# Kernel optimization log

Hardware: AMD Instinct MI355X
Metric: run time of the kernel (lower is better)

The kernel has to match this reference:

```python
import jax, jax.numpy as jnp
import numpy as np

D_MODEL = 512
NUM_HEADS = 8


def setup_inputs() -> dict:
    key = jax.random.key(0)
    ks = jax.random.split(key, 6)
    B, S, D = 4, 2048, D_MODEL
    Q = jax.random.normal(ks[0], (B, S, D), dtype=jnp.float32)
    K = jax.random.normal(ks[1], (B, S, D), dtype=jnp.float32)
    V = jax.random.normal(ks[2], (B, S, D), dtype=jnp.float32)
    # boolean mask, True = masked out; random so no row is fully masked
    mask = jax.random.randint(ks[3], (B, S, S), 0, 2).astype(jnp.bool_)
    scale = 1.0 / np.sqrt(D)
    Wq = jax.random.normal(ks[4], (D, D), dtype=jnp.float32) * scale
    Wo = jax.random.normal(ks[5], (D, D), dtype=jnp.float32) * scale
    return {"Q": Q, "K": K, "V": V, "mask": mask, "Wq": Wq, "Wo": Wo}


def reference(Q, K, V, mask, Wq, Wo):
    B, S, D = Q.shape
    H = NUM_HEADS
    dk = D // H
    # Faithful to the source: Q_Linear's weight (Wq) is applied to Q, K AND V
    # (K_Linear / V_Linear are dead parameters in the original module).
    q = (Q @ Wq.T).reshape(B, S, H, dk)
    k = (K @ Wq.T).reshape(B, S, H, dk)
    v = (V @ Wq.T).reshape(B, S, H, dk)
    # scores: [B, H, Sq, Sk]
    scores = jnp.einsum("bqhd,bkhd->bhqk", q, k)
    scores = jnp.where(mask[:, None, :, :], -jnp.inf, scores)
    w = jax.nn.softmax(scores / jnp.sqrt(jnp.asarray(dk, scores.dtype)), axis=-1)
    c = jnp.einsum("bhqk,bkhd->bqhd", w, v).reshape(B, S, D)
    return c @ Wo.T
```

## Files before the change

kernel.cpp:

```cpp
#include <hip/hip_runtime.h>
#include <math.h>

#define B_ 4
#define S_ 2048
#define D_ 512
#define H_ 8
#define DK_ 64
#define MROWS (B_ * S_)

typedef short bf16x8 __attribute__((ext_vector_type(8)));
typedef float f32x4 __attribute__((ext_vector_type(4)));
typedef float f32x16 __attribute__((ext_vector_type(16)));

static __device__ __forceinline__ unsigned short f2bf(float x) {
    unsigned int u = __float_as_uint(x);
    return (unsigned short)((u + 0x7FFFu + ((u >> 16) & 1u)) >> 16);
}
static __device__ __forceinline__ unsigned int cvt_pk_bf16(float a, float b) {
    unsigned int r;
    asm("v_cvt_pk_bf16_f32 %0, %1, %2" : "=v"(r) : "v"(a), "v"(b));
    return r;
}
static __device__ __forceinline__ float exp2_fast(float x) {
    float r;
    asm("v_exp_f32 %0, %1" : "=v"(r) : "v"(x));
    return r;
}
static __device__ __forceinline__ void gld_lds16(const unsigned short* g, unsigned short* l) {
    __builtin_amdgcn_global_load_lds(
        (const __attribute__((address_space(1))) unsigned int*)g,
        (__attribute__((address_space(3))) unsigned int*)l, 16, 0, 0);
}
static __device__ __forceinline__ void plswap(unsigned int& a, unsigned int& b) {
    asm volatile("v_permlane32_swap_b32 %0, %1" : "+v"(a), "+v"(b));
}

#define NXE (MROWS * D_)
#define NWE (D_ * D_)
#define CAST_BLOCKS ((3 * NXE + 2 * NWE) / 8 / 256)
#define MASKE (B_ * S_ * S_)
#define MASK_BLOCKS (MASKE / 256 / 4)
#define MASKB_BYTE (MASKE / 256 / 16)

__global__ __launch_bounds__(256) void prep(const float* __restrict__ Q,
                                            const float* __restrict__ K,
                                            const float* __restrict__ V,
                                            const float* __restrict__ Wq,
                                            const float* __restrict__ Wo,
                                            const void* __restrict__ mask,
                                            unsigned short* __restrict__ Qb,
                                            unsigned short* __restrict__ Kb,
                                            unsigned short* __restrict__ Vb,
                                            unsigned short* __restrict__ Wqb,
                                            unsigned short* __restrict__ Wob,
                                            unsigned long long* __restrict__ mb) {
    if (blockIdx.x < CAST_BLOCKS) {
        const int NA = NXE / 8;
        const int NWn = NWE / 8;
        int id = blockIdx.x * 256 + threadIdx.x;
        const float* src;
        unsigned short* dst;
        if (id < 3 * NA) {
            int a = id / NA, r = id - a * NA;
            src = (a == 0 ? Q : a == 1 ? K : V) + (size_t)r * 8;
            dst = (a == 0 ? Qb : a == 1 ? Kb : Vb) + (size_t)r * 8;
        } else {
            int r = id - 3 * NA;
            int a = r / NWn; r -= a * NWn;
            src = (a == 0 ? Wq : Wo) + (size_t)r * 8;
            dst = (a == 0 ? Wqb : Wob) + (size_t)r * 8;
        }
        float4 x = *(const float4*)src;
        float4 y = *(const float4*)(src + 4);
        unsigned short u[8] = {f2bf(x.x), f2bf(x.y), f2bf(x.z), f2bf(x.w),
                               f2bf(y.x), f2bf(y.y), f2bf(y.z), f2bf(y.w)};
        *(uint4*)dst = *(const uint4*)u;
    } else {
        const int mblk = blockIdx.x - CAST_BLOCKS;
        unsigned int accw = 0;
        if ((threadIdx.x & 63) == 0) {
            const unsigned int* mw0 = (const unsigned int*)mask;
            #pragma unroll
            for (int i = 0; i < 16; ++i) accw |= mw0[i];
        }
        accw = __shfl(accw, 0);
        const bool bytemode = (accw & 0xFFFFFF00u) != 0u;
        if (bytemode) {
            if (mblk >= MASKB_BYTE) return;
            const int gid = mblk * 256 + threadIdx.x;
            uint4 x = ((const uint4*)mask)[gid];
            unsigned int n[4];
            const unsigned int xs[4] = {x.x, x.y, x.z, x.w};
            #pragma unroll
            for (int i = 0; i < 4; ++i) {
                unsigned int y = xs[i];
                y |= y >> 4; y |= y >> 2; y |= y >> 1;
                y &= 0x01010101u;
                n[i] = (y * 0x01020408u) >> 24;
            }
            const unsigned short piece =
                (unsigned short)(n[0] | (n[1] << 4) | (n[2] << 8) | (n[3] << 12));
            ((unsigned short*)mb)[gid] = piece;
        } else {
            const int wid = (mblk * 256 + threadIdx.x) >> 6;
            const int lane = threadIdx.x & 63;
            const unsigned int* mi = (const unsigned int*)mask;
            const size_t base = (size_t)wid * 256;
            unsigned long long b0 = __ballot(mi[base + lane] != 0);
            unsigned long long b1 = __ballot(mi[base + 64 + lane] != 0);
            unsigned long long b2 = __ballot(mi[base + 128 + lane] != 0);
            unsigned long long b3 = __ballot(mi[base + 192 + lane] != 0);
            if (lane == 0) {
                const size_t wix = base >> 6;
                mb[wix] = b0; mb[wix + 1] = b1; mb[wix + 2] = b2; mb[wix + 3] = b3;
            }
        }
    }
}

__global__ __launch_bounds__(256) void proj3(const unsigned short* __restrict__ Qb,
                                             const unsigned short* __restrict__ Kb,
                                             const unsigned short* __restrict__ Vb,
                                             const unsigned short* __restrict__ Wqb,
                                             unsigned short* __restrict__ qs,
                                             unsigned short* __restrict__ kbo,
                                             unsigned short* __restrict__ vt) {
    __shared__ unsigned short smx[16384];
    const int t = threadIdx.x;
    const int w = t >> 6, lane = t & 63, col = lane & 15, quad = lane >> 4;
    const int bm = blockIdx.x * 128, bn = blockIdx.y * 128;
    const int z = blockIdx.z;
    const unsigned short* X = (z == 0) ? Qb : (z == 1) ? Kb : Vb;
    const int wm = (w >> 1) * 64, wn = (w & 1) * 64;

    const int sr = w * 32 + (lane >> 2);
    const int ssw = (((lane & 3) ^ ((lane >> 3) & 3)) * 8);
    const unsigned short* ags = X + (size_t)(bm + sr) * D_ + ssw;
    const unsigned short* bgs = Wqb + (size_t)(bn + sr) * D_ + ssw;
    const int pseg = ((quad ^ ((col >> 1) & 3)) * 8);

    f32x4 acc[4][4];
    #pragma unroll
    for (int i = 0; i < 4; ++i)
        #pragma unroll
        for (int j = 0; j < 4; ++j) acc[i][j] = (f32x4){0.f, 0.f, 0.f, 0.f};

    gld_lds16(ags, &smx[w * 1024]);
    gld_lds16(ags + 16 * D_, &smx[w * 1024 + 512]);
    gld_lds16(bgs, &smx[4096 + w * 1024]);
    gld_lds16(bgs + 16 * D_, &smx[4096 + w * 1024 + 512]);
    __asm__ __volatile__("s_waitcnt vmcnt(0)" ::: "memory");
    __builtin_amdgcn_s_barrier();

    int cur = 0;
    #pragma unroll 1
    for (int k0 = 0; k0 < D_; k0 += 32) {
        if (k0 + 32 < D_) {
            const int nb = (cur ^ 1) * 8192;
            gld_lds16(ags + k0 + 32, &smx[nb + w * 1024]);
            gld_lds16(ags + 16 * D_ + k0 + 32, &smx[nb + w * 1024 + 512]);
            gld_lds16(bgs + k0 + 32, &smx[nb + 4096 + w * 1024]);
            gld_lds16(bgs + 16 * D_ + k0 + 32, &smx[nb + 4096 + w * 1024 + 512]);
        }
        __builtin_amdgcn_sched_barrier(0);

        const int cb = cur * 8192;
        bf16x8 af[4], bg[4];
        #pragma unroll
        for (int i = 0; i < 4; ++i)
            af[i] = *(const bf16x8*)&smx[cb + (wm + i * 16 + col) * 32 + pseg];
        #pragma unroll
        for (int j = 0; j < 4; ++j)
            bg[j] = *(const bf16x8*)&smx[cb + 4096 + (wn + j * 16 + col) * 32 + pseg];
        #pragma unroll
        for (int i = 0; i < 4; ++i)
            #pragma unroll
            for (int j = 0; j < 4; ++j)
                acc[i][j] = __builtin_amdgcn_mfma_f32_16x16x32_bf16(
                    af[i], bg[j], acc[i][j], 0, 0, 0);

        __asm__ __volatile__("s_waitcnt vmcnt(0)" ::: "memory");
        __builtin_amdgcn_s_barrier();
        cur ^= 1;
    }

    if (z == 2) {
        #pragma unroll
        for (int i = 0; i < 4; ++i) {
            const int R = bm + wm + i * 16 + quad * 4;
            const int bb = R >> 11, s0 = R & (S_ - 1);
            #pragma unroll
            for (int j = 0; j < 4; ++j) {
                const int C = bn + wn + j * 16 + col;
                const int hh = C >> 6, dd = C & (DK_ - 1);
                ushort4 u = make_ushort4(f2bf(acc[i][j][0]), f2bf(acc[i][j][1]),
                                         f2bf(acc[i][j][2]), f2bf(acc[i][j][3]));
                *(ushort4*)&vt[(((size_t)bb * H_ + hh) * DK_ + dd) * S_ + s0] = u;
            }
        }
    } else {
        unsigned short* O = (z == 0) ? qs : kbo;
        const float scl = (z == 0) ? 0.18033688f : 1.0f;
        #pragma unroll
        for (int i = 0; i < 4; ++i)
            #pragma unroll
            for (int j = 0; j < 4; ++j) {
                const int R = bm + wm + i * 16 + quad * 4;
                const int C = bn + wn + j * 16 + col;
                #pragma unroll
                for (int r = 0; r < 4; ++r)
                    O[(size_t)(R + r) * D_ + C] = f2bf(acc[i][j][r] * scl);
            }
    }
}

__global__ __launch_bounds__(256) void gemm_out(const unsigned short* __restrict__ Xb,
                                                const unsigned short* __restrict__ Wob,
                                                float* __restrict__ Out) {
    __shared__ unsigned short smx[16384];
    const int t = threadIdx.x;
    const int w = t >> 6, lane = t & 63, col = lane & 15, quad = lane >> 4;
    const int bm = blockIdx.x * 128, bn = blockIdx.y * 128;
    const int wm = (w >> 1) * 64, wn = (w & 1) * 64;

    const int sr = w * 32 + (lane >> 2);
    const int ssw = (((lane & 3) ^ ((lane >> 3) & 3)) * 8);
    const unsigned short* ags = Xb + (size_t)(bm + sr) * D_ + ssw;
    const unsigned short* bgs = Wob + (size_t)(bn + sr) * D_ + ssw;
    const int pseg = ((quad ^ ((col >> 1) & 3)) * 8);

    f32x4 acc[4][4];
    #pragma unroll
    for (int i = 0; i < 4; ++i)
        #pragma unroll
        for (int j = 0; j < 4; ++j) acc[i][j] = (f32x4){0.f, 0.f, 0.f, 0.f};

    gld_lds16(ags, &smx[w * 1024]);
    gld_lds16(ags + 16 * D_, &smx[w * 1024 + 512]);
    gld_lds16(bgs, &smx[4096 + w * 1024]);
    gld_lds16(bgs + 16 * D_, &smx[4096 + w * 1024 + 512]);
    __asm__ __volatile__("s_waitcnt vmcnt(0)" ::: "memory");
    __builtin_amdgcn_s_barrier();

    int cur = 0;
    #pragma unroll 1
    for (int k0 = 0; k0 < D_; k0 += 32) {
        if (k0 + 32 < D_) {
            const int nb = (cur ^ 1) * 8192;
            gld_lds16(ags + k0 + 32, &smx[nb + w * 1024]);
            gld_lds16(ags + 16 * D_ + k0 + 32, &smx[nb + w * 1024 + 512]);
            gld_lds16(bgs + k0 + 32, &smx[nb + 4096 + w * 1024]);
            gld_lds16(bgs + 16 * D_ + k0 + 32, &smx[nb + 4096 + w * 1024 + 512]);
        }
        __builtin_amdgcn_sched_barrier(0);

        const int cb = cur * 8192;
        bf16x8 af[4], bg[4];
        #pragma unroll
        for (int i = 0; i < 4; ++i)
            af[i] = *(const bf16x8*)&smx[cb + (wm + i * 16 + col) * 32 + pseg];
        #pragma unroll
        for (int j = 0; j < 4; ++j)
            bg[j] = *(const bf16x8*)&smx[cb + 4096 + (wn + j * 16 + col) * 32 + pseg];
        #pragma unroll
        for (int i = 0; i < 4; ++i)
            #pragma unroll
            for (int j = 0; j < 4; ++j)
                acc[i][j] = __builtin_amdgcn_mfma_f32_16x16x32_bf16(
                    af[i], bg[j], acc[i][j], 0, 0, 0);

        __asm__ __volatile__("s_waitcnt vmcnt(0)" ::: "memory");
        __builtin_amdgcn_s_barrier();
        cur ^= 1;
    }

    #pragma unroll
    for (int i = 0; i < 4; ++i)
        #pragma unroll
        for (int j = 0; j < 4; ++j) {
            const int R = bm + wm + i * 16 + quad * 4;
            const int C = bn + wn + j * 16 + col;
            #pragma unroll
            for (int r = 0; r < 4; ++r)
                Out[(size_t)(R + r) * D_ + C] = acc[i][j][r];
        }
}

__global__ __launch_bounds__(256, 4) void attn_mfma(
        const unsigned short* __restrict__ qb,
        const unsigned short* __restrict__ kb,
        const unsigned short* __restrict__ vt,
        const unsigned long long* __restrict__ mb,
        unsigned short* __restrict__ o0,
        unsigned short* __restrict__ o1,
        float* __restrict__ l0,
        float* __restrict__ l1) {
    __shared__ unsigned short sm[16384];
    const int t = threadIdx.x;
    const int w = t >> 6;
    const int lane = t & 63;
    const int q5 = lane & 31;
    const int hi = lane >> 5;
    const int h = blockIdx.y;
    const int b = blockIdx.z >> 1;
    const int khalf = blockIdx.z & 1;
    const int bh = b * H_ + h;
    const int qrow0 = blockIdx.x * 128 + w * 32;

    unsigned short* opart = khalf ? o1 : o0;
    float* lpart = khalf ? l1 : l0;

    const unsigned int chk = cvt_pk_bf16(1.0f, 2.0f);
    const bool ablow = ((chk & 0xFFFFu) == 0x3F80u);

    bf16x8 qf[4];
    {
        const unsigned short* qp =
            qb + (size_t)(b * S_ + qrow0 + q5) * D_ + h * DK_ + hi * 8;
        #pragma unroll
        for (int dsl = 0; dsl < 4; ++dsl)
            qf[dsl] = *(const bf16x8*)(qp + dsl * 16);
    }

    bf16x8 ones8;
    #pragma unroll
    for (int i = 0; i < 8; ++i) ones8[i] = (short)0x3F80;

    const float CREF = 8.656170245f;
    f32x16 Oa, Ob, lacc, crefv;
    #pragma unroll
    for (int i = 0; i < 16; ++i) {
        Oa[i] = 0.f; Ob[i] = 0.f; lacc[i] = 0.f; crefv[i] = -CREF;
    }

    const int kbeg = khalf * (S_ / 2);

    const int ln8 = lane >> 3;
    const int fs8 = ((lane & 7) ^ ln8) * 8;
    const int r0 = w * 16 + ln8;
    const unsigned short* pK0 = kb + (size_t)(b * S_ + kbeg + r0) * D_ + h * DK_ + fs8;
    const unsigned short* pK1 = pK0 + 8 * D_;
    const unsigned short* pV0 = vt + ((size_t)bh * DK_ + r0) * S_ + kbeg + fs8;
    const unsigned short* pV1 = pV0 + 8 * S_;

    const unsigned long long* mbase =
        mb + (size_t)(b * S_ + qrow0 + q5) * (S_ / 64) + (kbeg >> 6);

    gld_lds16(pK0, &sm[w * 1024]);
    gld_lds16(pK1, &sm[w * 1024 + 512]);
    gld_lds16(pV0, &sm[4096 + w * 1024]);
    gld_lds16(pV1, &sm[4096 + w * 1024 + 512]);
    pK0 += 64 * D_; pK1 += 64 * D_; pV0 += 64; pV1 += 64;

    const int x7 = (q5 & 7);

    #pragma unroll 1
    for (int ti = 0; ti < 16; ++ti) {
        unsigned long long mw = mbase[ti];
        __builtin_amdgcn_sched_barrier(0);
        if (ti < 15) {
            const int nb = (ti & 1) ? 0 : 8192;
            gld_lds16(pK0, &sm[nb + w * 1024]);
            gld_lds16(pK1, &sm[nb + w * 1024 + 512]);
            gld_lds16(pV0, &sm[nb + 4096 + w * 1024]);
            gld_lds16(pV1, &sm[nb + 4096 + w * 1024 + 512]);
            pK0 += 64 * D_; pK1 += 64 * D_; pV0 += 64; pV1 += 64;
            __asm__ __volatile__("s_waitcnt vmcnt(5)" ::: "memory");
        } else {
            __asm__ __volatile__("s_waitcnt vmcnt(1)" ::: "memory");
        }
        __builtin_amdgcn_s_barrier();

        const int KB = (ti & 1) ? 8192 : 0;
        const int VB = KB + 4096;
        const unsigned long long msh = mw >> (hi * 4);

        #pragma unroll
        for (int kbi = 0; kbi < 2; ++kbi) {
            const int krow = KB + (kbi * 32 + q5) * 64;
            __builtin_amdgcn_s_setprio(1);
            bf16x8 kf0 = *(const bf16x8*)&sm[krow + ((hi) ^ x7) * 8];
            f32x16 S = __builtin_amdgcn_mfma_f32_32x32x16_bf16(kf0, qf[0], crefv, 0, 0, 0);
            #pragma unroll
            for (int dsl = 1; dsl < 4; ++dsl) {
                bf16x8 kf = *(const bf16x8*)&sm[krow + (((dsl << 1) | hi) ^ x7) * 8];
                S = __builtin_amdgcn_mfma_f32_32x32x16_bf16(kf, qf[dsl], S, 0, 0, 0);
            }
            __builtin_amdgcn_s_setprio(0);

            float p[16];
            #pragma unroll
            for (int r = 0; r < 16; ++r) {
                const int c = kbi * 32 + (r & 3) + 8 * (r >> 2);
                const bool msk = ((msh >> c) & 1ull) != 0ull;
                p[r] = exp2_fast(msk ? -1e30f : S[r]);
            }

            #pragma unroll
            for (int ksl = 0; ksl < 2; ++ksl) {
                const int bsl = ksl * 8;
                unsigned int uA = ablow ? cvt_pk_bf16(p[bsl], p[bsl + 1])
                                        : cvt_pk_bf16(p[bsl + 1], p[bsl]);
                unsigned int uB = ablow ? cvt_pk_bf16(p[bsl + 2], p[bsl + 3])
                                        : cvt_pk_bf16(p[bsl + 3], p[bsl + 2]);
                unsigned int uC = ablow ? cvt_pk_bf16(p[bsl + 4], p[bsl + 5])
                                        : cvt_pk_bf16(p[bsl + 5], p[bsl + 4]);
                unsigned int uD = ablow ? cvt_pk_bf16(p[bsl + 6], p[bsl + 7])
                                        : cvt_pk_bf16(p[bsl + 7], p[bsl + 6]);
                plswap(uA, uC);
                plswap(uB, uD);
                union { unsigned int u[4]; bf16x8 v; } pa;
                pa.u[0] = uA; pa.u[1] = uB; pa.u[2] = uC; pa.u[3] = uD;

                const int slice = kbi * 2 + ksl;
                const int vseg = (((slice << 1) | hi) ^ x7) * 8;
                bf16x8 vf0 = *(const bf16x8*)&sm[VB + q5 * 64 + vseg];
                bf16x8 vf1 = *(const bf16x8*)&sm[VB + (32 + q5) * 64 + vseg];
                __builtin_amdgcn_s_setprio(1);
                lacc = __builtin_amdgcn_mfma_f32_32x32x16_bf16(pa.v, ones8, lacc, 0, 0, 0);
                Oa = __builtin_amdgcn_mfma_f32_32x32x16_bf16(pa.v, vf0, Oa, 0, 0, 0);
                Ob = __builtin_amdgcn_mfma_f32_32x32x16_bf16(pa.v, vf1, Ob, 0, 0, 0);
                __builtin_amdgcn_s_setprio(0);
            }
        }

        __builtin_amdgcn_s_barrier();
    }

    #pragma unroll
    for (int r = 0; r < 16; ++r) {
        const int qq = (r & 3) + 8 * (r >> 2) + 4 * hi;
        const size_t row = (size_t)(b * S_ + qrow0 + qq);
        opart[row * D_ + h * DK_ + q5]      = f2bf(Oa[r]);
        opart[row * D_ + h * DK_ + 32 + q5] = f2bf(Ob[r]);
        if (q5 == 0) lpart[row * H_ + h] = lacc[r];
    }
}

__global__ __launch_bounds__(256) void combine(const unsigned short* __restrict__ o0,
                                               const unsigned short* __restrict__ o1,
                                               const float* __restrict__ l0,
                                               const float* __restrict__ l1,
                                               unsigned short* __restrict__ cb) {
    const int id = blockIdx.x * 256 + threadIdx.x;
    const size_t base = (size_t)id * 8;
    const int row = (int)(base >> 9);
    const int hh = ((int)base & (D_ - 1)) >> 6;
    uint4 ua = *(const uint4*)(o0 + base);
    uint4 ub = *(const uint4*)(o1 + base);
    const float inv = 1.0f / (l0[(size_t)row * H_ + hh] + l1[(size_t)row * H_ + hh]);
    const unsigned short* pa = (const unsigned short*)&ua;
    const unsigned short* pb = (const unsigned short*)&ub;
    unsigned short out[8];
    #pragma unroll
    for (int i = 0; i < 8; ++i) {
        float fa = __uint_as_float((unsigned int)pa[i] << 16);
        float fb = __uint_as_float((unsigned int)pb[i] << 16);
        out[i] = f2bf((fa + fb) * inv);
    }
    *(uint4*)(cb + base) = *(const uint4*)out;
}

extern "C" void kernel_launch(void* const* d_in, const int* in_sizes, int n_in,
                              void* d_out, int out_size, void* d_ws, size_t ws_size,
                              hipStream_t stream) {
    const float* Q    = (const float*)d_in[0];
    const float* K    = (const float*)d_in[1];
    const float* V    = (const float*)d_in[2];
    const void*  mask = d_in[3];
    const float* Wq   = (const float*)d_in[4];
    const float* Wo   = (const float*)d_in[5];
    float* out = (float*)d_out;

    const size_t NX = (size_t)MROWS * D_;
    const size_t NW = (size_t)D_ * D_;
    unsigned short* Qb   = (unsigned short*)d_ws;
    unsigned short* Kb   = Qb + NX;
    unsigned short* Vb   = Kb + NX;
    unsigned short* Wqb  = Vb + NX;
    unsigned short* Wob  = Wqb + NW;
    unsigned short* qbuf = Wob + NW;
    unsigned short* kbuf = qbuf + NX;
    unsigned short* vtb  = kbuf + NX;
    unsigned short* cbuf = vtb + NX;
    unsigned long long* mb = (unsigned long long*)(cbuf + NX);

    unsigned short* o0 = Qb;
    unsigned short* o1 = Kb;
    float* l0 = (float*)Vb;
    float* l1 = l0 + (size_t)MROWS * H_;

    prep<<<dim3(CAST_BLOCKS + MASK_BLOCKS), dim3(256), 0, stream>>>(
        Q, K, V, Wq, Wo, mask, Qb, Kb, Vb, Wqb, Wob, mb);

    proj3<<<dim3(MROWS / 128, D_ / 128, 3), dim3(256), 0, stream>>>(
        Qb, Kb, Vb, Wqb, qbuf, kbuf, vtb);

    attn_mfma<<<dim3(S_ / 128, H_, B_ * 2), dim3(256), 0, stream>>>(
        qbuf, kbuf, vtb, mb, o0, o1, l0, l1);

    combine<<<dim3((int)(NX / 8 / 256)), dim3(256), 0, stream>>>(o0, o1, l0, l1, cbuf);

    gemm_out<<<dim3(MROWS / 128, D_ / 128), dim3(256), 0, stream>>>(cbuf, Wob, out);
}
```

Baseline: 244.3 us.

## Fuse split-KV combine into output GEMM and triple-buffer projection loads

Removes the separate combine kernel by having gemm_out load both partial attention outputs and the softmax denominators, normalize and convert to bf16 in registers, and stage the result into LDS as the A operand. The B operand (Wo) moves to a three-stage LDS ring with prefetch distance two. The proj3 GEMM likewise moves to a three-stage LDS ring, waiting on vmcnt(4) instead of draining all loads each step. This cuts one launch and the write and re-read of the combined buffer. In exchange gemm_out does redundant normalization work across its column blocks and needs more LDS per block.

```diff
diff --git a/kernel.cpp b/kernel.cpp
--- a/kernel.cpp
+++ b/kernel.cpp
@@ -125,7 +125,7 @@
                                              unsigned short* __restrict__ qs,
                                              unsigned short* __restrict__ kbo,
                                              unsigned short* __restrict__ vt) {
-    __shared__ unsigned short smx[16384];
+    __shared__ unsigned short smx[24576];
     const int t = threadIdx.x;
     const int w = t >> 6, lane = t & 63, col = lane & 15, quad = lane >> 4;
     const int bm = blockIdx.x * 128, bn = blockIdx.y * 128;
@@ -145,26 +145,30 @@
         #pragma unroll
         for (int j = 0; j < 4; ++j) acc[i][j] = (f32x4){0.f, 0.f, 0.f, 0.f};
 
-    gld_lds16(ags, &smx[w * 1024]);
-    gld_lds16(ags + 16 * D_, &smx[w * 1024 + 512]);
-    gld_lds16(bgs, &smx[4096 + w * 1024]);
-    gld_lds16(bgs + 16 * D_, &smx[4096 + w * 1024 + 512]);
-    __asm__ __volatile__("s_waitcnt vmcnt(0)" ::: "memory");
+    #pragma unroll
+    for (int s = 0; s < 2; ++s) {
+        const int bb = s * 8192;
+        gld_lds16(ags + s * 32, &smx[bb + w * 1024]);
+        gld_lds16(ags + 16 * D_ + s * 32, &smx[bb + w * 1024 + 512]);
+        gld_lds16(bgs + s * 32, &smx[bb + 4096 + w * 1024]);
+        gld_lds16(bgs + 16 * D_ + s * 32, &smx[bb + 4096 + w * 1024 + 512]);
+    }
+    __asm__ __volatile__("s_waitcnt vmcnt(4)" ::: "memory");
     __builtin_amdgcn_s_barrier();
 
-    int cur = 0;
     #pragma unroll 1
-    for (int k0 = 0; k0 < D_; k0 += 32) {
-        if (k0 + 32 < D_) {
-            const int nb = (cur ^ 1) * 8192;
-            gld_lds16(ags + k0 + 32, &smx[nb + w * 1024]);
-            gld_lds16(ags + 16 * D_ + k0 + 32, &smx[nb + w * 1024 + 512]);
-            gld_lds16(bgs + k0 + 32, &smx[nb + 4096 + w * 1024]);
-            gld_lds16(bgs + 16 * D_ + k0 + 32, &smx[nb + 4096 + w * 1024 + 512]);
+    for (int ts = 0; ts < 16; ++ts) {
+        if (ts + 2 < 16) {
+            const int nb = ((ts + 2) % 3) * 8192;
+            const int ko = (ts + 2) * 32;
+            gld_lds16(ags + ko, &smx[nb + w * 1024]);
+            gld_lds16(ags + 16 * D_ + ko, &smx[nb + w * 1024 + 512]);
+            gld_lds16(bgs + ko, &smx[nb + 4096 + w * 1024]);
+            gld_lds16(bgs + 16 * D_ + ko, &smx[nb + 4096 + w * 1024 + 512]);
         }
         __builtin_amdgcn_sched_barrier(0);
 
-        const int cb = cur * 8192;
+        const int cb = (ts % 3) * 8192;
         bf16x8 af[4], bg[4];
         #pragma unroll
         for (int i = 0; i < 4; ++i)
@@ -179,9 +183,12 @@
                 acc[i][j] = __builtin_amdgcn_mfma_f32_16x16x32_bf16(
                     af[i], bg[j], acc[i][j], 0, 0, 0);
 
-        __asm__ __volatile__("s_waitcnt vmcnt(0)" ::: "memory");
-        __builtin_amdgcn_s_barrier();
-        cur ^= 1;
+        if (ts < 14) {
+            __asm__ __volatile__("s_waitcnt vmcnt(4)" ::: "memory");
+        } else if (ts == 14) {
+            __asm__ __volatile__("s_waitcnt vmcnt(0)" ::: "memory");
+        }
+        if (ts < 15) __builtin_amdgcn_s_barrier();
     }
 
     if (z == 2) {
@@ -214,10 +221,14 @@
     }
 }
 
-__global__ __launch_bounds__(256) void gemm_out(const unsigned short* __restrict__ Xb,
+__global__ __launch_bounds__(256) void gemm_out(const unsigned short* __restrict__ o0,
+                                                const unsigned short* __restrict__ o1,
+                                                const float* __restrict__ l0,
+                                                const float* __restrict__ l1,
                                                 const unsigned short* __restrict__ Wob,
                                                 float* __restrict__ Out) {
-    __shared__ unsigned short smx[16384];
+    __shared__ unsigned short smx[20480];
+    __shared__ float invt[128 * 8];
     const int t = threadIdx.x;
     const int w = t >> 6, lane = t & 63, col = lane & 15, quad = lane >> 4;
     const int bm = blockIdx.x * 128, bn = blockIdx.y * 128;
@@ -225,7 +236,8 @@
 
     const int sr = w * 32 + (lane >> 2);
     const int ssw = (((lane & 3) ^ ((lane >> 3) & 3)) * 8);
-    const unsigned short* ags = Xb + (size_t)(bm + sr) * D_ + ssw;
+    const unsigned short* ag0 = o0 + (size_t)(bm + sr) * D_ + ssw;
+    const unsigned short* ag1 = o1 + (size_t)(bm + sr) * D_ + ssw;
     const unsigned short* bgs = Wob + (size_t)(bn + sr) * D_ + ssw;
     const int pseg = ((quad ^ ((col >> 1) & 3)) * 8);
 
@@ -235,33 +247,78 @@
         #pragma unroll
         for (int j = 0; j < 4; ++j) acc[i][j] = (f32x4){0.f, 0.f, 0.f, 0.f};
 
-    gld_lds16(ags, &smx[w * 1024]);
-    gld_lds16(ags + 16 * D_, &smx[w * 1024 + 512]);
-    gld_lds16(bgs, &smx[4096 + w * 1024]);
-    gld_lds16(bgs + 16 * D_, &smx[4096 + w * 1024 + 512]);
-    __asm__ __volatile__("s_waitcnt vmcnt(0)" ::: "memory");
+    gld_lds16(bgs, &smx[8192 + w * 1024]);
+    gld_lds16(bgs + 16 * D_, &smx[8192 + w * 1024 + 512]);
+    uint4 p00 = *(const uint4*)(ag0);
+    uint4 p01 = *(const uint4*)(ag1);
+    uint4 p10 = *(const uint4*)(ag0 + 16 * D_);
+    uint4 p11 = *(const uint4*)(ag1 + 16 * D_);
+    gld_lds16(bgs + 32, &smx[12288 + w * 1024]);
+    gld_lds16(bgs + 16 * D_ + 32, &smx[12288 + w * 1024 + 512]);
+
+    #pragma unroll
+    for (int i = 0; i < 4; ++i) {
+        const int e = t * 4 + i;
+        const int row = bm + (e >> 3), hh = e & 7;
+        invt[e] = 1.0f / (l0[(size_t)row * H_ + hh] + l1[(size_t)row * H_ + hh]);
+    }
+    __asm__ __volatile__("s_waitcnt lgkmcnt(0)" ::: "memory");
     __builtin_amdgcn_s_barrier();
 
-    int cur = 0;
+    {
+        const float ivA = invt[sr * 8];
+        const float ivB = invt[(sr + 16) * 8];
+        const unsigned short* pa = (const unsigned short*)&p00;
+        const unsigned short* pb = (const unsigned short*)&p01;
+        unsigned short ob[8];
+        #pragma unroll
+        for (int i = 0; i < 8; ++i) {
+            float fa = __uint_as_float((unsigned int)pa[i] << 16);
+            float fb = __uint_as_float((unsigned int)pb[i] << 16);
+            ob[i] = f2bf((fa + fb) * ivA);
+        }
+        *(uint4*)&smx[w * 1024 + lane * 8] = *(const uint4*)ob;
+        pa = (const unsigned short*)&p10;
+        pb = (const unsigned short*)&p11;
+        #pragma unroll
+        for (int i = 0; i < 8; ++i) {
+            float fa = __uint_as_float((unsigned int)pa[i] << 16);
+            float fb = __uint_as_float((unsigned int)pb[i] << 16);
+            ob[i] = f2bf((fa + fb) * ivB);
+        }
+        *(uint4*)&smx[w * 1024 + 512 + lane * 8] = *(const uint4*)ob;
+    }
+    __asm__ __volatile__("s_waitcnt lgkmcnt(0)" ::: "memory");
+    __builtin_amdgcn_s_barrier();
+
     #pragma unroll 1
-    for (int k0 = 0; k0 < D_; k0 += 32) {
-        if (k0 + 32 < D_) {
-            const int nb = (cur ^ 1) * 8192;
-            gld_lds16(ags + k0 + 32, &smx[nb + w * 1024]);
-            gld_lds16(ags + 16 * D_ + k0 + 32, &smx[nb + w * 1024 + 512]);
-            gld_lds16(bgs + k0 + 32, &smx[nb + 4096 + w * 1024]);
-            gld_lds16(bgs + 16 * D_ + k0 + 32, &smx[nb + 4096 + w * 1024 + 512]);
+    for (int ts = 0; ts < 16; ++ts) {
+        uint4 a00, a01, a10, a11;
+        const bool hasA = (ts + 1 < 16);
+        if (hasA) {
+            const int ko = (ts + 1) * 32;
+            a00 = *(const uint4*)(ag0 + ko);
+            a01 = *(const uint4*)(ag1 + ko);
+            a10 = *(const uint4*)(ag0 + 16 * D_ + ko);
+            a11 = *(const uint4*)(ag1 + 16 * D_ + ko);
+        }
+        if (ts + 2 < 16) {
+            const int bb = 8192 + ((ts + 2) % 3) * 4096;
+            const int ko = (ts + 2) * 32;
+            gld_lds16(bgs + ko, &smx[bb + w * 1024]);
+            gld_lds16(bgs + 16 * D_ + ko, &smx[bb + w * 1024 + 512]);
         }
         __builtin_amdgcn_sched_barrier(0);
 
-        const int cb = cur * 8192;
+        const int ab = (ts & 1) * 4096;
+        const int bb = 8192 + (ts % 3) * 4096;
         bf16x8 af[4], bg[4];
         #pragma unroll
         for (int i = 0; i < 4; ++i)
-            af[i] = *(const bf16x8*)&smx[cb + (wm + i * 16 + col) * 32 + pseg];
+            af[i] = *(const bf16x8*)&smx[ab + (wm + i * 16 + col) * 32 + pseg];
         #pragma unroll
         for (int j = 0; j < 4; ++j)
-            bg[j] = *(const bf16x8*)&smx[cb + 4096 + (wn + j * 16 + col) * 32 + pseg];
+            bg[j] = *(const bf16x8*)&smx[bb + (wn + j * 16 + col) * 32 + pseg];
         #pragma unroll
         for (int i = 0; i < 4; ++i)
             #pragma unroll
@@ -269,9 +326,33 @@
                 acc[i][j] = __builtin_amdgcn_mfma_f32_16x16x32_bf16(
                     af[i], bg[j], acc[i][j], 0, 0, 0);
 
-        __asm__ __volatile__("s_waitcnt vmcnt(0)" ::: "memory");
-        __builtin_amdgcn_s_barrier();
-        cur ^= 1;
+        if (hasA) {
+            const int hh = (ts + 1) >> 1;
+            const float ivA = invt[sr * 8 + hh];
+            const float ivB = invt[(sr + 16) * 8 + hh];
+            const int na = ((ts + 1) & 1) * 4096;
+            const unsigned short* pa = (const unsigned short*)&a00;
+            const unsigned short* pb = (const unsigned short*)&a01;
+            unsigned short ob[8];
+            #pragma unroll
+            for (int i = 0; i < 8; ++i) {
+                float fa = __uint_as_float((unsigned int)pa[i] << 16);
+                float fb = __uint_as_float((unsigned int)pb[i] << 16);
+                ob[i] = f2bf((fa + fb) * ivA);
+            }
+            *(uint4*)&smx[na + w * 1024 + lane * 8] = *(const uint4*)ob;
+            pa = (const unsigned short*)&a10;
+            pb = (const unsigned short*)&a11;
+            #pragma unroll
+            for (int i = 0; i < 8; ++i) {
+                float fa = __uint_as_float((unsigned int)pa[i] << 16);
+                float fb = __uint_as_float((unsigned int)pb[i] << 16);
+                ob[i] = f2bf((fa + fb) * ivB);
+            }
+            *(uint4*)&smx[na + w * 1024 + 512 + lane * 8] = *(const uint4*)ob;
+        }
+        __asm__ __volatile__("s_waitcnt lgkmcnt(0)" ::: "memory");
+        if (ts < 15) __builtin_amdgcn_s_barrier();
     }
 
     #pragma unroll
@@ -437,30 +518,6 @@
     }
 }
 
-__global__ __launch_bounds__(256) void combine(const unsigned short* __restrict__ o0,
-                                               const unsigned short* __restrict__ o1,
-                                               const float* __restrict__ l0,
-                                               const float* __restrict__ l1,
-                                               unsigned short* __restrict__ cb) {
-    const int id = blockIdx.x * 256 + threadIdx.x;
-    const size_t base = (size_t)id * 8;
-    const int row = (int)(base >> 9);
-    const int hh = ((int)base & (D_ - 1)) >> 6;
-    uint4 ua = *(const uint4*)(o0 + base);
-    uint4 ub = *(const uint4*)(o1 + base);
-    const float inv = 1.0f / (l0[(size_t)row * H_ + hh] + l1[(size_t)row * H_ + hh]);
-    const unsigned short* pa = (const unsigned short*)&ua;
-    const unsigned short* pb = (const unsigned short*)&ub;
-    unsigned short out[8];
-    #pragma unroll
-    for (int i = 0; i < 8; ++i) {
-        float fa = __uint_as_float((unsigned int)pa[i] << 16);
-        float fb = __uint_as_float((unsigned int)pb[i] << 16);
-        out[i] = f2bf((fa + fb) * inv);
-    }
-    *(uint4*)(cb + base) = *(const uint4*)out;
-}
-
 extern "C" void kernel_launch(void* const* d_in, const int* in_sizes, int n_in,
                               void* d_out, int out_size, void* d_ws, size_t ws_size,
                               hipStream_t stream) {
@@ -499,7 +556,6 @@
     attn_mfma<<<dim3(S_ / 128, H_, B_ * 2), dim3(256), 0, stream>>>(
         qbuf, kbuf, vtb, mb, o0, o1, l0, l1);
 
-    combine<<<dim3((int)(NX / 8 / 256)), dim3(256), 0, stream>>>(o0, o1, l0, l1, cbuf);
-
-    gemm_out<<<dim3(MROWS / 128, D_ / 128), dim3(256), 0, stream>>>(cbuf, Wob, out);
-}
+    gemm_out<<<dim3(MROWS / 128, D_ / 128), dim3(256), 0, stream>>>(
+        o0, o1, l0, l1, Wob, out);
+}
```

Measured after the change: 246.4 us. Within noise of the previous version (+0.9%).
